# Optimization experiments

Hardware: AMD Instinct MI355X
Metric: run time of the kernel (lower is better)

Reference implementation:

```python
import jax, jax.numpy as jnp
import numpy as np

H = 512  # hidden_size
IN = 512  # input_size


def setup_inputs() -> dict:
    key = jax.random.key(0)
    ks = jax.random.split(key, 11)
    s = 1.0 / np.sqrt(H)
    T, B = 512, 256
    return {
        "x": jax.random.normal(ks[0], (T, B, IN), jnp.float32),
        "h0": jnp.zeros((B, H), jnp.float32),
        "g0": jnp.zeros((B, H), jnp.float32),
        # torch nn.Linear convention: y = x @ W.T + b, W ~ U(-1/sqrt(fan_in), ..)
        "Wx": jax.random.uniform(ks[1], (4 * H, IN), jnp.float32, -s, s),
        "bx": jax.random.uniform(ks[2], (4 * H,), jnp.float32, -s, s),
        "Wh": jax.random.uniform(ks[3], (3 * H, H), jnp.float32, -s, s),
        "bh": jax.random.uniform(ks[4], (3 * H,), jnp.float32, -s, s),
        "Wgh": jax.random.uniform(ks[5], (3 * H, H), jnp.float32, -s, s),
        "bgh": jax.random.uniform(ks[6], (3 * H,), jnp.float32, -s, s),
        "Whd": jax.random.uniform(ks[7], (3 * H, H), jnp.float32, -s, s),
        "bhd": jax.random.uniform(ks[8], (3 * H,), jnp.float32, -s, s),
        "Wg": jax.random.uniform(ks[9], (2 * H, H), jnp.float32, -s, s),
        "bg": jax.random.uniform(ks[10], (2 * H,), jnp.float32, -s, s),
    }


def _split(a, n):
    return jnp.split(a, n, axis=-1)


def reference(x, h0, g0, Wx, bx, Wh, bh, Wgh, bgh, Whd, bhd, Wg, bg):
    def step(carry, x_t):
        h, g = carry
        x_z, x_r, x_h, x_u = _split(x_t @ Wx.T + bx, 4)
        h_z, h_r, h_u = _split(h @ Wh.T + bh, 3)
        g_z, g_r, g_u = _split(g @ Wgh.T + bgh, 3)
        z = jax.nn.sigmoid(x_z + h_z + g_z)
        r = jax.nn.sigmoid(x_r + h_r + g_r)
        u = jax.nn.sigmoid(x_u + h_u + g_u)
        h_new = (1 - z) * h + z * jnp.tanh(x_h + r * h + u * g)
        h_d = h_new - h
        g_z2, g_r2 = _split(g @ Wg.T + bg, 2)
        hd_z, hd_r, hd_g = _split(h_d @ Whd.T + bhd, 3)
        z2 = jax.nn.sigmoid(hd_z + g_z2)
        r2 = jax.nn.sigmoid(hd_r + g_r2)
        g_new = (1 - z2) * g + z2 * jnp.tanh(hd_g + r2 * g)
        return (h_new, g_new), h_new

    (h, g), hs = jax.lax.scan(step, (h0, g0), x)
    return hs, h[None], g[None]
```

## Files before the change

### kernel.cpp

```cpp
#include <hip/hip_runtime.h>

#define Tn 512
#define Bn 256
#define Hn 512
#define INn 512
#define TPB 512

typedef __attribute__((ext_vector_type(8))) short bf16x8;
typedef __attribute__((ext_vector_type(4))) float f32x4;

__device__ __forceinline__ unsigned short f2bf(float f) {
  unsigned int u = __float_as_uint(f);
  unsigned int r = (u + 0x7fffu + ((u >> 16) & 1u)) >> 16;
  return (unsigned short)r;
}

__device__ __forceinline__ float sigm(float x) { return 1.0f / (1.0f + __expf(-x)); }
__device__ __forceinline__ float tanh_f(float x) { return 2.0f / (1.0f + __expf(-2.0f * x)) - 1.0f; }

__device__ __forceinline__ bf16x8 ld8(const unsigned short* p) {
  return *reinterpret_cast<const bf16x8*>(p);
}

__device__ __forceinline__ unsigned long long ald8(const unsigned short* p) {
  return __hip_atomic_load((const unsigned long long*)p, __ATOMIC_RELAXED,
                           __HIP_MEMORY_SCOPE_AGENT);
}
__device__ __forceinline__ bf16x8 ald16(const unsigned short* p) {
  union { unsigned long long u[2]; bf16x8 v; } r;
  r.u[0] = ald8(p);
  r.u[1] = ald8(p + 4);
  return r.v;
}
__device__ __forceinline__ void ast4(unsigned short* p, unsigned int v) {
  __hip_atomic_store((unsigned int*)p, v, __ATOMIC_RELAXED, __HIP_MEMORY_SCOPE_AGENT);
}

__device__ __forceinline__ f32x4 mfma16(bf16x8 a, bf16x8 b, f32x4 c) {
  return __builtin_amdgcn_mfma_f32_16x16x32_bf16(a, b, c, 0, 0, 0);
}

__global__ __launch_bounds__(256) void cvt_kernel(const float* __restrict__ in,
                                                  unsigned short* __restrict__ out, int n) {
  const int stride = gridDim.x * blockDim.x * 4;
  for (int i = (blockIdx.x * blockDim.x + threadIdx.x) * 4; i < n; i += stride) {
    float4 v = *reinterpret_cast<const float4*>(in + i);
    ushort4 o;
    o.x = f2bf(v.x); o.y = f2bf(v.y); o.z = f2bf(v.z); o.w = f2bf(v.w);
    *reinterpret_cast<ushort4*>(out + i) = o;
  }
}

__global__ __launch_bounds__(256) void xp_gemm_kernel(
    const unsigned short* __restrict__ xb,
    const unsigned short* __restrict__ Wxb,
    const float* __restrict__ bx,
    const float* __restrict__ bh,
    const float* __restrict__ bgh,
    float* __restrict__ XP) {
  const int m0 = blockIdx.x * 64;
  const int n0 = blockIdx.y * 64;
  const int wave = threadIdx.x >> 6;
  const int lane = threadIdx.x & 63;
  const int l15 = lane & 15;
  const int lk = (lane >> 4) * 8;
  const int ro = (wave >> 1) * 32;
  const int co = (wave & 1) * 32;
  const unsigned short* ap = xb + (size_t)(m0 + ro + l15) * INn + lk;
  const unsigned short* bp = Wxb + (size_t)(n0 + co + l15) * INn + lk;
  f32x4 acc[2][2] = {};
  for (int k = 0; k < INn; k += 32) {
    bf16x8 a0 = ld8(ap + k);
    bf16x8 a1 = ld8(ap + 16 * INn + k);
    bf16x8 w0 = ld8(bp + k);
    bf16x8 w1 = ld8(bp + 16 * INn + k);
    acc[0][0] = mfma16(a0, w0, acc[0][0]);
    acc[0][1] = mfma16(a0, w1, acc[0][1]);
    acc[1][0] = mfma16(a1, w0, acc[1][0]);
    acc[1][1] = mfma16(a1, w1, acc[1][1]);
  }
#pragma unroll
  for (int rt = 0; rt < 2; ++rt)
#pragma unroll
    for (int ct = 0; ct < 2; ++ct) {
      const int col = n0 + co + ct * 16 + l15;
      float bias = bx[col];
      if (col < 1024) bias += bh[col] + bgh[col];
      else if (col >= 1536) bias += bh[col - 512] + bgh[col - 512];
#pragma unroll
      for (int r = 0; r < 4; ++r) {
        const int row = m0 + ro + rt * 16 + (lane >> 4) * 4 + r;
        XP[(size_t)row * 2048 + col] = acc[rt][ct][r] + bias;
      }
    }
}

__device__ __forceinline__ void group_barrier(unsigned int* cnt, unsigned int target) {
  __syncthreads();
  if (threadIdx.x == 0) {
    __hip_atomic_fetch_add(cnt, 1u, __ATOMIC_RELAXED, __HIP_MEMORY_SCOPE_AGENT);
    while (__hip_atomic_load(cnt, __ATOMIC_RELAXED, __HIP_MEMORY_SCOPE_AGENT) < target)
      __builtin_amdgcn_s_sleep(1);
  }
  __syncthreads();
}

__device__ __forceinline__ void stage_A(const unsigned short* src,
                                        unsigned short* dst_l, int b0, int tid) {
  const int rr = tid >> 4;
  const int cu = (tid & 15) * 8;
  const unsigned short* s = src + (size_t)(b0 + rr) * Hn + cu * 4;
  char* dbase = (char*)dst_l + rr * 1024;
  const int swz = (rr & 7) << 4;
#pragma unroll
  for (int q = 0; q < 8; ++q) {
    unsigned long long v = ald8(s + q * 4);
    *(unsigned long long*)(dbase + (((cu + q) * 8) ^ swz)) = v;
  }
}

__global__ __launch_bounds__(512, 1) void persist_kernel(
    const unsigned short* __restrict__ Whb,
    const unsigned short* __restrict__ Wghb,
    const unsigned short* __restrict__ Whdb,
    const unsigned short* __restrict__ Wgb,
    const float* __restrict__ XP,
    const float* __restrict__ bhd,
    const float* __restrict__ bg,
    unsigned short* __restrict__ hb0,
    unsigned short* __restrict__ gb,
    unsigned short* __restrict__ hdb,
    float* __restrict__ g_master,
    const float* __restrict__ h0,
    const float* __restrict__ g0,
    float* __restrict__ hs,
    float* __restrict__ h_tail,
    float* __restrict__ g_tail,
    unsigned int* __restrict__ barcnt,
    int t0, int Tc) {
  __shared__ unsigned short Wh_l[48 * 512];
  __shared__ unsigned short Wgh_l[48 * 512];
  __shared__ unsigned short As_l[32 * 512];
  __shared__ float pa[8][32][17];
  __shared__ float xp_l[4][32][17];

  const int tid = threadIdx.x;
  const int grp = blockIdx.x & 7;
  const int jblk = blockIdx.x >> 3;
  const int j0 = jblk * 16;
  const int b0 = grp * 32;
  const int wv = tid >> 6;
  const int lane = tid & 63;
  const int l15 = lane & 15;
  const int lk = (lane >> 4) * 8;
  unsigned int* cnt = barcnt + grp;

  for (int i = tid; i < 48 * 64; i += TPB) {
    const int rr = i >> 6, c = i & 63;
    const int grow = (rr >> 4) * 512 + j0 + (rr & 15);
    const int byte = rr * 1024 + ((c * 16) ^ ((rr & 7) << 4));
    *reinterpret_cast<uint4*>(reinterpret_cast<char*>(Wh_l) + byte) =
        *reinterpret_cast<const uint4*>(Whb + (size_t)grow * 512 + c * 8);
    *reinterpret_cast<uint4*>(reinterpret_cast<char*>(Wgh_l) + byte) =
        *reinterpret_cast<const uint4*>(Wghb + (size_t)grow * 512 + c * 8);
  }

  const int bl_e = tid >> 4, jl_e = tid & 15;
  const int j_e = j0 + jl_e;
  const size_t o_e = (size_t)(b0 + bl_e) * Hn + j_e;
  float h_m = (t0 == 0) ? h0[o_e] : hs[(size_t)(t0 - 1) * (Bn * Hn) + o_e];
  float g_m = (t0 == 0) ? g0[o_e] : g_master[o_e];
  const float bz2 = bhd[j_e] + bg[j_e];
  const float br2 = bhd[512 + j_e] + bg[512 + j_e];
  const float bgc = bhd[1024 + j_e];

  for (int i = tid; i < 2048; i += TPB) {
    const int gate = i >> 9, bb = (i >> 4) & 31, jj = i & 15;
    xp_l[gate][bb][jj] = XP[(size_t)(b0 + bb) * 2048 + gate * 512 + j0 + jj];
  }
  __syncthreads();

  unsigned int nbar = 0;
  float z2p = 0.0f, r2p = 0.0f;
  const int swzA = (l15 & 7) << 4;

  for (int tt = 0; tt < Tc; ++tt) {
    const int t = t0 + tt;
    const unsigned short* hb_cur = hb0 + (size_t)(t & 1) * (Bn * Hn);
    unsigned short* hb_nxt = hb0 + (size_t)((t + 1) & 1) * (Bn * Hn);

    stage_A(gb, As_l, b0, tid);
    __syncthreads();

    if (wv == 0) {
      const unsigned short* ap0 = hb_cur + (size_t)(b0 + l15) * Hn + lk;
      f32x4 acc[2][3] = {};
      for (int kt = 0; kt < 16; ++kt) {
        const int k = kt * 32;
        bf16x8 a0 = ald16(ap0 + k);
        bf16x8 a1 = ald16(ap0 + 16 * Hn + k);
#pragma unroll
        for (int s = 0; s < 3; ++s) {
          const int rr = s * 16 + l15;
          const int byte = rr * 1024 + (((k + lk) * 2) ^ swzA);
          bf16x8 bf = *reinterpret_cast<const bf16x8*>(
              reinterpret_cast<const char*>(Wh_l) + byte);
          acc[0][s] = mfma16(a0, bf, acc[0][s]);
          acc[1][s] = mfma16(a1, bf, acc[1][s]);
        }
      }
#pragma unroll
      for (int s = 0; s < 3; ++s)
#pragma unroll
        for (int rt = 0; rt < 2; ++rt)
#pragma unroll
          for (int r = 0; r < 4; ++r)
            pa[s][rt * 16 + (lane >> 4) * 4 + r][l15] = acc[rt][s][r];
    } else if (wv == 1) {
      f32x4 acc[2][3] = {};
      for (int kt = 0; kt < 16; ++kt) {
        const int k = kt * 32;
        const int abyte = (((k + lk) * 2) ^ swzA);
        bf16x8 a0 = *reinterpret_cast<const bf16x8*>(
            reinterpret_cast<const char*>(As_l) + l15 * 1024 + abyte);
        bf16x8 a1 = *reinterpret_cast<const bf16x8*>(
            reinterpret_cast<const char*>(As_l) + (16 + l15) * 1024 + abyte);
#pragma unroll
        for (int s = 0; s < 3; ++s) {
          const int rr = s * 16 + l15;
          const int byte = rr * 1024 + (((k + lk) * 2) ^ swzA);
          bf16x8 bf = *reinterpret_cast<const bf16x8*>(
              reinterpret_cast<const char*>(Wgh_l) + byte);
          acc[0][s] = mfma16(a0, bf, acc[0][s]);
          acc[1][s] = mfma16(a1, bf, acc[1][s]);
        }
      }
#pragma unroll
      for (int s = 0; s < 3; ++s)
#pragma unroll
        for (int rt = 0; rt < 2; ++rt)
#pragma unroll
          for (int r = 0; r < 4; ++r)
            pa[3 + s][rt * 16 + (lane >> 4) * 4 + r][l15] = acc[rt][s][r];
    } else if (wv == 2) {
      const unsigned short* bp0 = Wgb + (size_t)(j0 + l15) * Hn + lk;
      const unsigned short* bp1 = Wgb + (size_t)(512 + j0 + l15) * Hn + lk;
      f32x4 acc[2][2] = {};
      for (int kt = 0; kt < 16; ++kt) {
        const int k = kt * 32;
        const int abyte = (((k + lk) * 2) ^ swzA);
        bf16x8 a0 = *reinterpret_cast<const bf16x8*>(
            reinterpret_cast<const char*>(As_l) + l15 * 1024 + abyte);
        bf16x8 a1 = *reinterpret_cast<const bf16x8*>(
            reinterpret_cast<const char*>(As_l) + (16 + l15) * 1024 + abyte);
        bf16x8 w0 = ld8(bp0 + k);
        bf16x8 w1 = ld8(bp1 + k);
        acc[0][0] = mfma16(a0, w0, acc[0][0]);
        acc[1][0] = mfma16(a1, w0, acc[1][0]);
        acc[0][1] = mfma16(a0, w1, acc[0][1]);
        acc[1][1] = mfma16(a1, w1, acc[1][1]);
      }
#pragma unroll
      for (int s = 0; s < 2; ++s)
#pragma unroll
        for (int rt = 0; rt < 2; ++rt)
#pragma unroll
          for (int r = 0; r < 4; ++r)
            pa[6 + s][rt * 16 + (lane >> 4) * 4 + r][l15] = acc[rt][s][r];
    }
    __syncthreads();

    {
      const float z = sigm(xp_l[0][bl_e][jl_e] + pa[0][bl_e][jl_e] + pa[3][bl_e][jl_e]);
      const float r = sigm(xp_l[1][bl_e][jl_e] + pa[1][bl_e][jl_e] + pa[4][bl_e][jl_e]);
      const float u = sigm(xp_l[3][bl_e][jl_e] + pa[2][bl_e][jl_e] + pa[5][bl_e][jl_e]);
      const float cand = tanh_f(xp_l[2][bl_e][jl_e] + r * h_m + u * g_m);
      const float hn = (1.0f - z) * h_m + z * cand;
      const float hd = hn - h_m;
      hs[(size_t)t * (Bn * Hn) + o_e] = hn;
      if (t == Tn - 1) h_tail[o_e] = hn;
      const unsigned int hn_u = f2bf(hn), hd_u = f2bf(hd);
      const unsigned int hn_hi = (unsigned int)__shfl_down((int)hn_u, 1);
      const unsigned int hd_hi = (unsigned int)__shfl_down((int)hd_u, 1);
      if ((jl_e & 1) == 0) {
        ast4(hb_nxt + o_e, hn_u | (hn_hi << 16));
        ast4(hdb + o_e, hd_u | (hd_hi << 16));
      }
      h_m = hn;
      z2p = pa[6][bl_e][jl_e];
      r2p = pa[7][bl_e][jl_e];
    }
    group_barrier(cnt, 32u * (++nbar));

    stage_A(hdb, As_l, b0, tid);
    __syncthreads();

    if (wv < 3) {
      const unsigned short* bp0 = Whdb + (size_t)(wv * 512 + j0 + l15) * Hn + lk;
      f32x4 acc[2] = {};
      for (int kt = 0; kt < 16; ++kt) {
        const int k = kt * 32;
        const int abyte = (((k + lk) * 2) ^ swzA);
        bf16x8 a0 = *reinterpret_cast<const bf16x8*>(
            reinterpret_cast<const char*>(As_l) + l15 * 1024 + abyte);
        bf16x8 a1 = *reinterpret_cast<const bf16x8*>(
            reinterpret_cast<const char*>(As_l) + (16 + l15) * 1024 + abyte);
        bf16x8 w0 = ld8(bp0 + k);
        acc[0] = mfma16(a0, w0, acc[0]);
        acc[1] = mfma16(a1, w0, acc[1]);
      }
#pragma unroll
      for (int rt = 0; rt < 2; ++rt)
#pragma unroll
        for (int r = 0; r < 4; ++r)
          pa[wv][rt * 16 + (lane >> 4) * 4 + r][l15] = acc[rt][r];
    } else if (tt + 1 < Tc) {
      for (int i = tid - 192; i < 2048; i += 320) {
        const int gate = i >> 9, bb = (i >> 4) & 31, jj = i & 15;
        xp_l[gate][bb][jj] =
            XP[(size_t)((tt + 1) * Bn + b0 + bb) * 2048 + gate * 512 + j0 + jj];
      }
    }
    __syncthreads();

    {
      const float z2 = sigm(pa[0][bl_e][jl_e] + z2p + bz2);
      const float r2 = sigm(pa[1][bl_e][jl_e] + r2p + br2);
      const float gc = tanh_f(pa[2][bl_e][jl_e] + bgc + r2 * g_m);
      const float gn = (1.0f - z2) * g_m + z2 * gc;
      g_m = gn;
      if (t == Tn - 1) g_tail[o_e] = gn;
      const unsigned int gn_u = f2bf(gn);
      const unsigned int gn_hi = (unsigned int)__shfl_down((int)gn_u, 1);
      if ((jl_e & 1) == 0) ast4(gb + o_e, gn_u | (gn_hi << 16));
    }
    group_barrier(cnt, 32u * (++nbar));
  }
  g_master[o_e] = g_m;
}

extern "C" void kernel_launch(void* const* d_in, const int* in_sizes, int n_in,
                              void* d_out, int out_size, void* d_ws, size_t ws_size,
                              hipStream_t stream) {
  const float* x   = (const float*)d_in[0];
  const float* h0  = (const float*)d_in[1];
  const float* g0  = (const float*)d_in[2];
  const float* Wx  = (const float*)d_in[3];
  const float* bx  = (const float*)d_in[4];
  const float* Wh  = (const float*)d_in[5];
  const float* bh  = (const float*)d_in[6];
  const float* Wgh = (const float*)d_in[7];
  const float* bgh = (const float*)d_in[8];
  const float* Whd = (const float*)d_in[9];
  const float* bhd = (const float*)d_in[10];
  const float* Wg  = (const float*)d_in[11];
  const float* bg  = (const float*)d_in[12];

  char* ws = (char*)d_ws;
  unsigned short* Whb  = (unsigned short*)(ws + 0);
  unsigned short* Wghb = (unsigned short*)(ws + 1572864);
  unsigned short* Whdb = (unsigned short*)(ws + 3145728);
  unsigned short* Wgb  = (unsigned short*)(ws + 4718592);
  unsigned short* Wxb  = (unsigned short*)(ws + 5767168);
  unsigned short* hb0  = (unsigned short*)(ws + 7864320);
  unsigned short* gb_  = (unsigned short*)(ws + 8388608);
  unsigned short* hdb  = (unsigned short*)(ws + 8650752);
  float* g_master      = (float*)(ws + 8912896);
  unsigned int* barcnt = (unsigned int*)(ws + 9437184);
  const size_t FIXED = 9453568ULL;

  int Tc = 64;
  while (Tc > 1 && FIXED + (size_t)Tc * (262144ULL + 2097152ULL) > ws_size) Tc >>= 1;
  unsigned short* xb = (unsigned short*)(ws + FIXED);
  float* XPc = (float*)(ws + FIXED + (size_t)Tc * 262144ULL);

  float* hs = (float*)d_out;
  float* h_tail = hs + (size_t)Tn * Bn * Hn;
  float* g_tail = h_tail + (size_t)Bn * Hn;

  hipMemsetAsync(barcnt, 0, 16384, stream);
  cvt_kernel<<<dim3(512), 256, 0, stream>>>(Wh, Whb, 1536 * 512);
  cvt_kernel<<<dim3(512), 256, 0, stream>>>(Wgh, Wghb, 1536 * 512);
  cvt_kernel<<<dim3(512), 256, 0, stream>>>(Whd, Whdb, 1536 * 512);
  cvt_kernel<<<dim3(512), 256, 0, stream>>>(Wg, Wgb, 1024 * 512);
  cvt_kernel<<<dim3(512), 256, 0, stream>>>(Wx, Wxb, 2048 * 512);
  cvt_kernel<<<dim3(128), 256, 0, stream>>>(h0, hb0, Bn * Hn);
  cvt_kernel<<<dim3(128), 256, 0, stream>>>(g0, gb_, Bn * Hn);

  const int nChunks = Tn / Tc;
  for (int c = 0; c < nChunks; ++c) {
    const int t0 = c * Tc;
    cvt_kernel<<<dim3(1024), 256, 0, stream>>>(x + (size_t)t0 * Bn * INn, xb,
                                               Tc * Bn * INn);
    xp_gemm_kernel<<<dim3(Tc * 4, 32), 256, 0, stream>>>(xb, Wxb, bx, bh, bgh, XPc);
    persist_kernel<<<dim3(256), dim3(TPB), 0, stream>>>(
        Whb, Wghb, Whdb, Wgb, XPc, bhd, bg, hb0, gb_, hdb, g_master, h0, g0,
        hs, h_tail, g_tail, barcnt + c * 8, t0, Tc);
  }
}
```

Baseline: 9.841 ms.

## Use per-block epoch flags barrier, bf16 tiled XP, and register-prefetched h operands

Replaces the atomic-counter group barrier with per-block epoch flags: each block stores its epoch and 32 lanes poll all flags in its group. XP is now stored in bf16 in a block-tiled layout, so each block fetches its step slice with contiguous 8-byte loads into double-buffered shared memory. Wave 0 prefetches the next h operand into registers right after the barrier instead of loading it at the start of the step, and g staging is spread across the other waves. This removes atomic contention and shortens the serial per-step critical path, but costs precision in XP and adds register pressure from the 64-entry rA array.

```diff
diff --git a/kernel.cpp b/kernel.cpp
--- a/kernel.cpp
+++ b/kernel.cpp
@@ -14,6 +14,9 @@
   unsigned int r = (u + 0x7fffu + ((u >> 16) & 1u)) >> 16;
   return (unsigned short)r;
 }
+__device__ __forceinline__ float bf2f(unsigned short u) {
+  return __uint_as_float(((unsigned int)u) << 16);
+}
 
 __device__ __forceinline__ float sigm(float x) { return 1.0f / (1.0f + __expf(-x)); }
 __device__ __forceinline__ float tanh_f(float x) { return 2.0f / (1.0f + __expf(-2.0f * x)) - 1.0f; }
@@ -25,12 +28,6 @@
 __device__ __forceinline__ unsigned long long ald8(const unsigned short* p) {
   return __hip_atomic_load((const unsigned long long*)p, __ATOMIC_RELAXED,
                            __HIP_MEMORY_SCOPE_AGENT);
-}
-__device__ __forceinline__ bf16x8 ald16(const unsigned short* p) {
-  union { unsigned long long u[2]; bf16x8 v; } r;
-  r.u[0] = ald8(p);
-  r.u[1] = ald8(p + 4);
-  return r.v;
 }
 __device__ __forceinline__ void ast4(unsigned short* p, unsigned int v) {
   __hip_atomic_store((unsigned int*)p, v, __ATOMIC_RELAXED, __HIP_MEMORY_SCOPE_AGENT);
@@ -57,7 +54,7 @@
     const float* __restrict__ bx,
     const float* __restrict__ bh,
     const float* __restrict__ bgh,
-    float* __restrict__ XP) {
+    unsigned short* __restrict__ XPb) {
   const int m0 = blockIdx.x * 64;
   const int n0 = blockIdx.y * 64;
   const int wave = threadIdx.x >> 6;
@@ -84,47 +81,58 @@
 #pragma unroll
     for (int ct = 0; ct < 2; ++ct) {
       const int col = n0 + co + ct * 16 + l15;
+      const int gate = col >> 9, jcol = col & 511;
+      const int jb = jcol >> 4, jl = jcol & 15;
       float bias = bx[col];
       if (col < 1024) bias += bh[col] + bgh[col];
       else if (col >= 1536) bias += bh[col - 512] + bgh[col - 512];
 #pragma unroll
       for (int r = 0; r < 4; ++r) {
         const int row = m0 + ro + rt * 16 + (lane >> 4) * 4 + r;
-        XP[(size_t)row * 2048 + col] = acc[rt][ct][r] + bias;
-      }
-    }
-}
-
-__device__ __forceinline__ void group_barrier(unsigned int* cnt, unsigned int target) {
+        const int ttl = row >> 8, bb = row & 255;
+        XPb[(((size_t)ttl * 8 + (bb >> 5)) * 32 + jb) * 2048 +
+            gate * 512 + (bb & 31) * 16 + jl] = f2bf(acc[rt][ct][r] + bias);
+      }
+    }
+}
+
+__device__ __forceinline__ void group_barrier(unsigned int* gflags, int jblk,
+                                              unsigned int epoch) {
   __syncthreads();
-  if (threadIdx.x == 0) {
-    __hip_atomic_fetch_add(cnt, 1u, __ATOMIC_RELAXED, __HIP_MEMORY_SCOPE_AGENT);
-    while (__hip_atomic_load(cnt, __ATOMIC_RELAXED, __HIP_MEMORY_SCOPE_AGENT) < target)
+  if (threadIdx.x < 64) {
+    if (threadIdx.x == 0)
+      __hip_atomic_store(gflags + jblk, epoch, __ATOMIC_RELAXED,
+                         __HIP_MEMORY_SCOPE_AGENT);
+    unsigned int* p = gflags + (threadIdx.x & 31);
+    while (__hip_atomic_load(p, __ATOMIC_RELAXED, __HIP_MEMORY_SCOPE_AGENT) < epoch)
       __builtin_amdgcn_s_sleep(1);
   }
   __syncthreads();
 }
 
-__device__ __forceinline__ void stage_A(const unsigned short* src,
-                                        unsigned short* dst_l, int b0, int tid) {
-  const int rr = tid >> 4;
-  const int cu = (tid & 15) * 8;
-  const unsigned short* s = src + (size_t)(b0 + rr) * Hn + cu * 4;
-  char* dbase = (char*)dst_l + rr * 1024;
-  const int swz = (rr & 7) << 4;
-#pragma unroll
-  for (int q = 0; q < 8; ++q) {
-    unsigned long long v = ald8(s + q * 4);
-    *(unsigned long long*)(dbase + (((cu + q) * 8) ^ swz)) = v;
-  }
-}
-
-__global__ __launch_bounds__(512, 1) void persist_kernel(
+__device__ __forceinline__ void stage_A_part(const unsigned short* src,
+                                             unsigned short* dst_l, int b0,
+                                             int idx0, int stride, int nIter) {
+  for (int q = 0; q < nIter; ++q) {
+    const int idx = idx0 + q * stride;
+    if (idx < 2048) {
+      const int rr = idx >> 6, c = idx & 63;
+      union { unsigned long long u[2]; uint4 v; } t;
+      const unsigned short* s = src + (size_t)(b0 + rr) * Hn + c * 8;
+      t.u[0] = ald8(s);
+      t.u[1] = ald8(s + 4);
+      *reinterpret_cast<uint4*>(reinterpret_cast<char*>(dst_l) + rr * 1024 +
+                                ((c * 16) ^ ((rr & 7) << 4))) = t.v;
+    }
+  }
+}
+
+__global__ __launch_bounds__(512, 2) void persist_kernel(
     const unsigned short* __restrict__ Whb,
     const unsigned short* __restrict__ Wghb,
     const unsigned short* __restrict__ Whdb,
     const unsigned short* __restrict__ Wgb,
-    const float* __restrict__ XP,
+    const unsigned short* __restrict__ XPb,
     const float* __restrict__ bhd,
     const float* __restrict__ bg,
     unsigned short* __restrict__ hb0,
@@ -136,13 +144,13 @@
     float* __restrict__ hs,
     float* __restrict__ h_tail,
     float* __restrict__ g_tail,
-    unsigned int* __restrict__ barcnt,
+    unsigned int* __restrict__ flags,
     int t0, int Tc) {
   __shared__ unsigned short Wh_l[48 * 512];
   __shared__ unsigned short Wgh_l[48 * 512];
   __shared__ unsigned short As_l[32 * 512];
   __shared__ float pa[8][32][17];
-  __shared__ float xp_l[4][32][17];
+  __shared__ unsigned short xp_ls[2][2048];
 
   const int tid = threadIdx.x;
   const int grp = blockIdx.x & 7;
@@ -153,7 +161,7 @@
   const int lane = tid & 63;
   const int l15 = lane & 15;
   const int lk = (lane >> 4) * 8;
-  unsigned int* cnt = barcnt + grp;
+  unsigned int* gflags = flags + grp * 32;
 
   for (int i = tid; i < 48 * 64; i += TPB) {
     const int rr = i >> 6, c = i & 63;
@@ -173,40 +181,65 @@
   const float bz2 = bhd[j_e] + bg[j_e];
   const float br2 = bhd[512 + j_e] + bg[512 + j_e];
   const float bgc = bhd[1024 + j_e];
-
-  for (int i = tid; i < 2048; i += TPB) {
-    const int gate = i >> 9, bb = (i >> 4) & 31, jj = i & 15;
-    xp_l[gate][bb][jj] = XP[(size_t)(b0 + bb) * 2048 + gate * 512 + j0 + jj];
+  const int xo = bl_e * 16 + jl_e;
+
+  {
+    const unsigned short* src = XPb + ((size_t)grp * 32 + jblk) * 2048;
+    *(unsigned long long*)&xp_ls[0][tid * 4] =
+        *(const unsigned long long*)(src + tid * 4);
+  }
+
+  unsigned long long rA[16][2][2];
+  if (wv == 0) {
+    const unsigned short* ap0 =
+        hb0 + (size_t)(t0 & 1) * (Bn * Hn) + (size_t)(b0 + l15) * Hn + lk;
+#pragma unroll
+    for (int kt = 0; kt < 16; ++kt) {
+      rA[kt][0][0] = ald8(ap0 + kt * 32);
+      rA[kt][0][1] = ald8(ap0 + kt * 32 + 4);
+      rA[kt][1][0] = ald8(ap0 + 16 * Hn + kt * 32);
+      rA[kt][1][1] = ald8(ap0 + 16 * Hn + kt * 32 + 4);
+    }
   }
   __syncthreads();
 
-  unsigned int nbar = 0;
+  unsigned int epoch = 0;
   float z2p = 0.0f, r2p = 0.0f;
   const int swzA = (l15 & 7) << 4;
 
   for (int tt = 0; tt < Tc; ++tt) {
     const int t = t0 + tt;
-    const unsigned short* hb_cur = hb0 + (size_t)(t & 1) * (Bn * Hn);
     unsigned short* hb_nxt = hb0 + (size_t)((t + 1) & 1) * (Bn * Hn);
-
-    stage_A(gb, As_l, b0, tid);
+    const int cur = tt & 1, nxt = (tt + 1) & 1;
+
+    if (wv >= 1) {
+      stage_A_part(gb, As_l, b0, tid - 64, 448, 5);
+      if (wv >= 3 && tt + 1 < Tc) {
+        const unsigned short* src =
+            XPb + (((size_t)(tt + 1) * 8 + grp) * 32 + jblk) * 2048;
+        for (int i = tid - 192; i < 512; i += 320)
+          *(unsigned long long*)&xp_ls[nxt][i * 4] =
+              *(const unsigned long long*)(src + i * 4);
+      }
+    }
     __syncthreads();
 
     if (wv == 0) {
-      const unsigned short* ap0 = hb_cur + (size_t)(b0 + l15) * Hn + lk;
       f32x4 acc[2][3] = {};
+#pragma unroll
       for (int kt = 0; kt < 16; ++kt) {
+        union { unsigned long long u[2]; bf16x8 v; } a0, a1;
+        a0.u[0] = rA[kt][0][0]; a0.u[1] = rA[kt][0][1];
+        a1.u[0] = rA[kt][1][0]; a1.u[1] = rA[kt][1][1];
         const int k = kt * 32;
-        bf16x8 a0 = ald16(ap0 + k);
-        bf16x8 a1 = ald16(ap0 + 16 * Hn + k);
 #pragma unroll
         for (int s = 0; s < 3; ++s) {
           const int rr = s * 16 + l15;
           const int byte = rr * 1024 + (((k + lk) * 2) ^ swzA);
-          bf16x8 bf = *reinterpret_cast<const bf16x8*>(
+          bf16x8 bw = *reinterpret_cast<const bf16x8*>(
               reinterpret_cast<const char*>(Wh_l) + byte);
-          acc[0][s] = mfma16(a0, bf, acc[0][s]);
-          acc[1][s] = mfma16(a1, bf, acc[1][s]);
+          acc[0][s] = mfma16(a0.v, bw, acc[0][s]);
+          acc[1][s] = mfma16(a1.v, bw, acc[1][s]);
         }
       }
 #pragma unroll
@@ -218,9 +251,10 @@
             pa[s][rt * 16 + (lane >> 4) * 4 + r][l15] = acc[rt][s][r];
     } else if (wv == 1) {
       f32x4 acc[2][3] = {};
+#pragma unroll
       for (int kt = 0; kt < 16; ++kt) {
         const int k = kt * 32;
-        const int abyte = (((k + lk) * 2) ^ swzA);
+        const int abyte = ((k + lk) * 2) ^ swzA;
         bf16x8 a0 = *reinterpret_cast<const bf16x8*>(
             reinterpret_cast<const char*>(As_l) + l15 * 1024 + abyte);
         bf16x8 a1 = *reinterpret_cast<const bf16x8*>(
@@ -229,10 +263,10 @@
         for (int s = 0; s < 3; ++s) {
           const int rr = s * 16 + l15;
           const int byte = rr * 1024 + (((k + lk) * 2) ^ swzA);
-          bf16x8 bf = *reinterpret_cast<const bf16x8*>(
+          bf16x8 bw = *reinterpret_cast<const bf16x8*>(
               reinterpret_cast<const char*>(Wgh_l) + byte);
-          acc[0][s] = mfma16(a0, bf, acc[0][s]);
-          acc[1][s] = mfma16(a1, bf, acc[1][s]);
+          acc[0][s] = mfma16(a0, bw, acc[0][s]);
+          acc[1][s] = mfma16(a1, bw, acc[1][s]);
         }
       }
 #pragma unroll
@@ -246,9 +280,10 @@
       const unsigned short* bp0 = Wgb + (size_t)(j0 + l15) * Hn + lk;
       const unsigned short* bp1 = Wgb + (size_t)(512 + j0 + l15) * Hn + lk;
       f32x4 acc[2][2] = {};
+#pragma unroll
       for (int kt = 0; kt < 16; ++kt) {
         const int k = kt * 32;
-        const int abyte = (((k + lk) * 2) ^ swzA);
+        const int abyte = ((k + lk) * 2) ^ swzA;
         bf16x8 a0 = *reinterpret_cast<const bf16x8*>(
             reinterpret_cast<const char*>(As_l) + l15 * 1024 + abyte);
         bf16x8 a1 = *reinterpret_cast<const bf16x8*>(
@@ -271,10 +306,10 @@
     __syncthreads();
 
     {
-      const float z = sigm(xp_l[0][bl_e][jl_e] + pa[0][bl_e][jl_e] + pa[3][bl_e][jl_e]);
-      const float r = sigm(xp_l[1][bl_e][jl_e] + pa[1][bl_e][jl_e] + pa[4][bl_e][jl_e]);
-      const float u = sigm(xp_l[3][bl_e][jl_e] + pa[2][bl_e][jl_e] + pa[5][bl_e][jl_e]);
-      const float cand = tanh_f(xp_l[2][bl_e][jl_e] + r * h_m + u * g_m);
+      const float z = sigm(bf2f(xp_ls[cur][xo]) + pa[0][bl_e][jl_e] + pa[3][bl_e][jl_e]);
+      const float r = sigm(bf2f(xp_ls[cur][512 + xo]) + pa[1][bl_e][jl_e] + pa[4][bl_e][jl_e]);
+      const float u = sigm(bf2f(xp_ls[cur][1536 + xo]) + pa[2][bl_e][jl_e] + pa[5][bl_e][jl_e]);
+      const float cand = tanh_f(bf2f(xp_ls[cur][1024 + xo]) + r * h_m + u * g_m);
       const float hn = (1.0f - z) * h_m + z * cand;
       const float hd = hn - h_m;
       hs[(size_t)t * (Bn * Hn) + o_e] = hn;
@@ -290,17 +325,18 @@
       z2p = pa[6][bl_e][jl_e];
       r2p = pa[7][bl_e][jl_e];
     }
-    group_barrier(cnt, 32u * (++nbar));
-
-    stage_A(hdb, As_l, b0, tid);
+    group_barrier(gflags, jblk, ++epoch);
+
+    stage_A_part(hdb, As_l, b0, tid, 512, 4);
     __syncthreads();
 
     if (wv < 3) {
       const unsigned short* bp0 = Whdb + (size_t)(wv * 512 + j0 + l15) * Hn + lk;
       f32x4 acc[2] = {};
+#pragma unroll
       for (int kt = 0; kt < 16; ++kt) {
         const int k = kt * 32;
-        const int abyte = (((k + lk) * 2) ^ swzA);
+        const int abyte = ((k + lk) * 2) ^ swzA;
         bf16x8 a0 = *reinterpret_cast<const bf16x8*>(
             reinterpret_cast<const char*>(As_l) + l15 * 1024 + abyte);
         bf16x8 a1 = *reinterpret_cast<const bf16x8*>(
@@ -314,11 +350,15 @@
 #pragma unroll
         for (int r = 0; r < 4; ++r)
           pa[wv][rt * 16 + (lane >> 4) * 4 + r][l15] = acc[rt][r];
-    } else if (tt + 1 < Tc) {
-      for (int i = tid - 192; i < 2048; i += 320) {
-        const int gate = i >> 9, bb = (i >> 4) & 31, jj = i & 15;
-        xp_l[gate][bb][jj] =
-            XP[(size_t)((tt + 1) * Bn + b0 + bb) * 2048 + gate * 512 + j0 + jj];
+    }
+    if (wv == 0 && tt + 1 < Tc) {
+      const unsigned short* ap0 = hb_nxt + (size_t)(b0 + l15) * Hn + lk;
+#pragma unroll
+      for (int kt = 0; kt < 16; ++kt) {
+        rA[kt][0][0] = ald8(ap0 + kt * 32);
+        rA[kt][0][1] = ald8(ap0 + kt * 32 + 4);
+        rA[kt][1][0] = ald8(ap0 + 16 * Hn + kt * 32);
+        rA[kt][1][1] = ald8(ap0 + 16 * Hn + kt * 32 + 4);
       }
     }
     __syncthreads();
@@ -334,7 +374,7 @@
       const unsigned int gn_hi = (unsigned int)__shfl_down((int)gn_u, 1);
       if ((jl_e & 1) == 0) ast4(gb + o_e, gn_u | (gn_hi << 16));
     }
-    group_barrier(cnt, 32u * (++nbar));
+    group_barrier(gflags, jblk, ++epoch);
   }
   g_master[o_e] = g_m;
 }
@@ -366,19 +406,19 @@
   unsigned short* gb_  = (unsigned short*)(ws + 8388608);
   unsigned short* hdb  = (unsigned short*)(ws + 8650752);
   float* g_master      = (float*)(ws + 8912896);
-  unsigned int* barcnt = (unsigned int*)(ws + 9437184);
+  unsigned int* flags  = (unsigned int*)(ws + 9437184);
   const size_t FIXED = 9453568ULL;
 
   int Tc = 64;
-  while (Tc > 1 && FIXED + (size_t)Tc * (262144ULL + 2097152ULL) > ws_size) Tc >>= 1;
-  unsigned short* xb = (unsigned short*)(ws + FIXED);
-  float* XPc = (float*)(ws + FIXED + (size_t)Tc * 262144ULL);
+  while (Tc > 1 && FIXED + (size_t)Tc * (262144ULL + 1048576ULL) > ws_size) Tc >>= 1;
+  unsigned short* xb  = (unsigned short*)(ws + FIXED);
+  unsigned short* XPb = (unsigned short*)(ws + FIXED + (size_t)Tc * 262144ULL);
 
   float* hs = (float*)d_out;
   float* h_tail = hs + (size_t)Tn * Bn * Hn;
   float* g_tail = h_tail + (size_t)Bn * Hn;
 
-  hipMemsetAsync(barcnt, 0, 16384, stream);
+  hipMemsetAsync(flags, 0, 16384, stream);
   cvt_kernel<<<dim3(512), 256, 0, stream>>>(Wh, Whb, 1536 * 512);
   cvt_kernel<<<dim3(512), 256, 0, stream>>>(Wgh, Wghb, 1536 * 512);
   cvt_kernel<<<dim3(512), 256, 0, stream>>>(Whd, Whdb, 1536 * 512);
@@ -392,9 +432,9 @@
     const int t0 = c * Tc;
     cvt_kernel<<<dim3(1024), 256, 0, stream>>>(x + (size_t)t0 * Bn * INn, xb,
                                                Tc * Bn * INn);
-    xp_gemm_kernel<<<dim3(Tc * 4, 32), 256, 0, stream>>>(xb, Wxb, bx, bh, bgh, XPc);
+    xp_gemm_kernel<<<dim3(Tc * 4, 32), 256, 0, stream>>>(xb, Wxb, bx, bh, bgh, XPb);
     persist_kernel<<<dim3(256), dim3(TPB), 0, stream>>>(
-        Whb, Wghb, Whdb, Wgb, XPc, bhd, bg, hb0, gb_, hdb, g_master, h0, g0,
-        hs, h_tail, g_tail, barcnt + c * 8, t0, Tc);
-  }
-}
+        Whb, Wghb, Whdb, Wgb, XPb, bhd, bg, hb0, gb_, hdb, g_master, h0, g0,
+        hs, h_tail, g_tail, flags + c * 256, t0, Tc);
+  }
+}
```

Measured after the change: 9.088 ms. -7.7%, faster.
